# Kernel tuning notes

Hardware: AMD Instinct MI355X
Metric: run time of the kernel (lower is better)

Reference implementation:

```python
import jax, jax.numpy as jnp
import numpy as np
from jax import lax

N = 8388608
HYP2F1_TERMS = 200  # z <= ~0.87 here, 0.87^200 ~ 1e-12 -> fully converged


def hyp2f1(p, q, s, z, n_terms=HYP2F1_TERMS):
    """Gauss 2F1(p, q; s; z) via its power series (|z|<1), fixed-length scan."""
    def step(carry, k):
        term, acc = carry
        term = term * (p + k) * (q + k) / ((s + k) * (k + 1.0)) * z
        return (term, acc + term), None
    ones = jnp.ones_like(z)
    (_, acc), _ = lax.scan(step, (ones, ones),
                           jnp.arange(n_terms, dtype=z.dtype))
    return acc


def setup_inputs() -> dict:
    key = jax.random.key(0)
    k1, k2, k3 = jax.random.split(key, 3)
    x = jax.random.randint(k1, (N,), 0, 20).astype(jnp.int32)
    T = jax.random.uniform(k2, (N,), minval=20.0, maxval=60.0, dtype=jnp.float32)
    u = jax.random.uniform(k3, (N,), dtype=jnp.float32)
    # recency in [0.2*T, 0.9*T] so T - t_x > 0 and z bounded away from 1;
    # t_x = 0 for customers with no repeat transactions (x == 0).
    t_x = jnp.where(x == 0, 0.0, (0.2 + 0.7 * u) * T)
    return {
        "x": x,
        "t_x": t_x,
        "T": T,
        "log_r": jnp.log(jnp.float32(0.9)),
        "log_alpha": jnp.log(jnp.float32(4.0)),
        "log_a": jnp.log(jnp.float32(0.8)),
        "log_b": jnp.log(jnp.float32(2.5)),
    }


def reference(x, t_x, T, log_r, log_alpha, log_a, log_b):
    xf = x.astype(jnp.float32)
    r = jnp.exp(log_r)
    alpha = jnp.exp(log_alpha)
    a = jnp.exp(log_a)
    b = jnp.exp(log_b)

    log_alpha_T = jnp.log(alpha + T)

    # x == 0 branch
    ll0 = r * (jnp.log(alpha) - log_alpha_T) + (jnp.log(b) - jnp.log(a + b))

    # x > 0 branch (safe to evaluate everywhere: T - t_x > 0 for all rows)
    term1 = lax.lgamma(r + xf) - lax.lgamma(r) - lax.lgamma(xf + 1.0)
    term2 = r * (jnp.log(alpha) - log_alpha_T)
    term3 = xf * (jnp.log(T - t_x) - log_alpha_T)
    term4 = (jnp.log(a) + lax.lgamma(a + b) - lax.lgamma(a)
             - lax.lgamma(a + b + xf) + lax.lgamma(a + xf))
    z = (T - t_x) / (alpha + T)
    term5 = jnp.log(hyp2f1(r + xf, a * jnp.ones_like(xf), a + b + xf, z))
    ll1 = term1 + term2 + term3 + term4 + term5

    return jnp.where(x == 0, ll0, ll1)
```

## Files before the change

kernel.cpp:

```cpp
#include <hip/hip_runtime.h>
#include <hip/hip_fp16.h>


#define NX    20
#define MT    64
#define NQ    (MT / 4)
#define ROWH  68
#define BLOB_BYTES (128 + NX * ROWH * 2)

__global__ void bgnbd_setup(const float* __restrict__ plr,
                            const float* __restrict__ pla,
                            const float* __restrict__ plA,
                            const float* __restrict__ plb,
                            float* __restrict__ ws)
{
    const int t = threadIdx.x;
    const float log_r     = plr[0];
    const float log_alpha = pla[0];
    const float log_a     = plA[0];
    const float log_b     = plb[0];
    const float r     = expf(log_r);
    const float a     = expf(log_a);
    const float b     = expf(log_b);
    const float alpha = expf(log_alpha);

    if (t == 0) {
        ws[0] = r;
        ws[1] = log_alpha;
        ws[2] = log_b - logf(a + b);
        ws[3] = alpha;
        ws[4] = 0.f; ws[5] = 0.f; ws[6] = 0.f; ws[7] = 0.f;
        for (int i = 28; i < 32; ++i) ws[i] = 0.f;
    }
    if (t < NX) {
        const float xf = (float)t;
        ws[8 + t] = lgammaf(r + xf) - lgammaf(r) - lgammaf(xf + 1.f)
                  + log_a + lgammaf(a + b) - lgammaf(a)
                  - lgammaf(a + b + xf) + lgammaf(a + xf);
        __half* Dh = reinterpret_cast<__half*>(ws + 32);
        const float p = r + xf;
        const float s = a + b + xf;
        float D = 1.f;
        for (int m = 0; m < MT; ++m) {
            Dh[t * ROWH + m] = __float2half(D);
            const float k = (float)m;
            D = D * (p + k) * (a + k) / ((s + k) * (k + 1.f));
        }
        for (int m = MT; m < ROWH; ++m) Dh[t * ROWH + m] = __float2half(0.f);
    }
}

__global__ __launch_bounds__(256) void bgnbd_main(
    const int*   __restrict__ xp,
    const float* __restrict__ txp,
    const float* __restrict__ Tp,
    const float* __restrict__ ws,
    float*       __restrict__ out,
    int n4)
{
    __shared__ __align__(16) unsigned char blob[BLOB_BYTES];
    const int tid = threadIdx.x;
    {
        const uint4* src = reinterpret_cast<const uint4*>(ws);
        uint4*       dst = reinterpret_cast<uint4*>(blob);
        if (tid < BLOB_BYTES / 16) dst[tid] = src[tid];
    }
    __syncthreads();

    const float*  s_sc = reinterpret_cast<const float*>(blob);
    const float*  s_Cx = s_sc + 8;
    const __half* s_D  = reinterpret_cast<const __half*>(blob + 128);

    const float r         = s_sc[0];
    const float log_alpha = s_sc[1];
    const float ll0c      = s_sc[2];
    const float alpha     = s_sc[3];

    const int gid = blockIdx.x * 256 + tid;
    if (gid >= n4) return;

    const int4   xv  = reinterpret_cast<const int4*>(xp)[gid];
    const float4 txv = reinterpret_cast<const float4*>(txp)[gid];
    const float4 Tv  = reinterpret_cast<const float4*>(Tp)[gid];

    int   xi[4]  = {xv.x, xv.y, xv.z, xv.w};
    float txa[4] = {txv.x, txv.y, txv.z, txv.w};
    float Ta[4]  = {Tv.x, Tv.y, Tv.z, Tv.w};

    float z[4], S[4], lat[4], Tm[4];
    int   xc[4];
    const __half* rowp[4];
    #pragma unroll
    for (int e = 0; e < 4; ++e) {
        const float aT = alpha + Ta[e];
        lat[e] = __logf(aT);
        Tm[e]  = Ta[e] - txa[e];
        z[e]   = __fdividef(Tm[e], aT);
        S[e]   = 0.f;
        int c = xi[e]; c = c < 0 ? 0 : (c > NX - 1 ? NX - 1 : c);
        xc[e]   = c;
        rowp[e] = s_D + c * ROWH;
    }

    #pragma unroll 4
    for (int g = NQ - 1; g >= 0; --g) {
        #pragma unroll
        for (int e = 0; e < 4; ++e) {
            const uint2 q = *reinterpret_cast<const uint2*>(rowp[e] + 4 * g);
            const __half2 h01 = __builtin_bit_cast(__half2, q.x);
            const __half2 h23 = __builtin_bit_cast(__half2, q.y);
            const float2 f01 = __half22float2(h01);
            const float2 f23 = __half22float2(h23);
            S[e] = fmaf(S[e], z[e], f23.y);
            S[e] = fmaf(S[e], z[e], f23.x);
            S[e] = fmaf(S[e], z[e], f01.y);
            S[e] = fmaf(S[e], z[e], f01.x);
        }
    }

    float res[4];
    #pragma unroll
    for (int e = 0; e < 4; ++e) {
        const float base = r * (log_alpha - lat[e]);
        const float xf   = (float)xi[e];
        const float ll1  = s_Cx[xc[e]] + base
                         + xf * (__logf(Tm[e]) - lat[e]) + __logf(S[e]);
        const float ll0  = base + ll0c;
        res[e] = (xi[e] == 0) ? ll0 : ll1;
    }
    reinterpret_cast<float4*>(out)[gid] = make_float4(res[0], res[1], res[2], res[3]);
}

extern "C" void kernel_launch(void* const* d_in, const int* in_sizes, int n_in,
                              void* d_out, int out_size, void* d_ws, size_t ws_size,
                              hipStream_t stream)
{
    const int*   xp  = (const int*)  d_in[0];
    const float* txp = (const float*)d_in[1];
    const float* Tp  = (const float*)d_in[2];
    const float* plr = (const float*)d_in[3];
    const float* pla = (const float*)d_in[4];
    const float* plA = (const float*)d_in[5];
    const float* plb = (const float*)d_in[6];
    float*       out = (float*)d_out;
    float*       ws  = (float*)d_ws;

    const int n  = in_sizes[0];
    const int n4 = n >> 2;
    const int grid = (n4 + 255) / 256;

    bgnbd_setup<<<1, 64, 0, stream>>>(plr, pla, plA, plb, ws);
    bgnbd_main<<<grid, 256, 0, stream>>>(xp, txp, Tp, ws, out, n4);
}
```

Before: 156.9 us.

## Halve hyp2f1 series terms and evaluate pairs with packed fp16 dot2

Cuts the per-element hypergeometric series from 64 to 32 stored coefficients. Evaluates them two at a time with v_dot2 (fdot2) against a packed (1, z) fp16 vector, with a z² Horner step. Folds r*log_alpha into the precomputed constants and moves the final logs to log2 form with a single ln2 rescale. The aim is to remove most of the per-element FMA and convert work in this compute-bound loop. The cost is accuracy: the series is truncated more aggressively, and z is rounded to fp16 inside the dot product.

```diff
diff --git a/kernel.cpp b/kernel.cpp
--- a/kernel.cpp
+++ b/kernel.cpp
@@ -3,10 +3,11 @@
 
 
 #define NX    20
-#define MT    64
-#define NQ    (MT / 4)
-#define ROWH  68
+#define MT    32
+#define ROWH  72
 #define BLOB_BYTES (128 + NX * ROWH * 2)
+
+typedef _Float16 half2_t __attribute__((ext_vector_type(2)));
 
 __global__ void bgnbd_setup(const float* __restrict__ plr,
                             const float* __restrict__ pla,
@@ -26,8 +27,8 @@
 
     if (t == 0) {
         ws[0] = r;
-        ws[1] = log_alpha;
-        ws[2] = log_b - logf(a + b);
+        ws[1] = 0.f;
+        ws[2] = r * log_alpha + log_b - logf(a + b);
         ws[3] = alpha;
         ws[4] = 0.f; ws[5] = 0.f; ws[6] = 0.f; ws[7] = 0.f;
         for (int i = 28; i < 32; ++i) ws[i] = 0.f;
@@ -36,7 +37,8 @@
         const float xf = (float)t;
         ws[8 + t] = lgammaf(r + xf) - lgammaf(r) - lgammaf(xf + 1.f)
                   + log_a + lgammaf(a + b) - lgammaf(a)
-                  - lgammaf(a + b + xf) + lgammaf(a + xf);
+                  - lgammaf(a + b + xf) + lgammaf(a + xf)
+                  + r * log_alpha;
         __half* Dh = reinterpret_cast<__half*>(ws + 32);
         const float p = r + xf;
         const float s = a + b + xf;
@@ -71,10 +73,9 @@
     const float*  s_Cx = s_sc + 8;
     const __half* s_D  = reinterpret_cast<const __half*>(blob + 128);
 
-    const float r         = s_sc[0];
-    const float log_alpha = s_sc[1];
-    const float ll0c      = s_sc[2];
-    const float alpha     = s_sc[3];
+    const float r     = s_sc[0];
+    const float ll0c  = s_sc[2];
+    const float alpha = s_sc[3];
 
     const int gid = blockIdx.x * 256 + tid;
     if (gid >= n4) return;
@@ -87,45 +88,46 @@
     float txa[4] = {txv.x, txv.y, txv.z, txv.w};
     float Ta[4]  = {Tv.x, Tv.y, Tv.z, Tv.w};
 
-    float z[4], S[4], lat[4], Tm[4];
-    int   xc[4];
+    float z[4], w[4], S[4], l2aT[4];
+    half2_t zp[4];
+    int xc[4];
     const __half* rowp[4];
     #pragma unroll
     for (int e = 0; e < 4; ++e) {
         const float aT = alpha + Ta[e];
-        lat[e] = __logf(aT);
-        Tm[e]  = Ta[e] - txa[e];
-        z[e]   = __fdividef(Tm[e], aT);
-        S[e]   = 0.f;
+        l2aT[e] = __log2f(aT);
+        const float Tm = Ta[e] - txa[e];
+        z[e] = __fdividef(Tm, aT);
+        w[e] = z[e] * z[e];
+        const unsigned zh = __half_as_ushort(__float2half(z[e]));
+        zp[e] = __builtin_bit_cast(half2_t, 0x3C00u | (zh << 16));
+        S[e] = 0.f;
         int c = xi[e]; c = c < 0 ? 0 : (c > NX - 1 ? NX - 1 : c);
         xc[e]   = c;
         rowp[e] = s_D + c * ROWH;
     }
 
-    #pragma unroll 4
-    for (int g = NQ - 1; g >= 0; --g) {
+    #pragma unroll
+    for (int j = 3; j >= 0; --j) {
         #pragma unroll
         for (int e = 0; e < 4; ++e) {
-            const uint2 q = *reinterpret_cast<const uint2*>(rowp[e] + 4 * g);
-            const __half2 h01 = __builtin_bit_cast(__half2, q.x);
-            const __half2 h23 = __builtin_bit_cast(__half2, q.y);
-            const float2 f01 = __half22float2(h01);
-            const float2 f23 = __half22float2(h23);
-            S[e] = fmaf(S[e], z[e], f23.y);
-            S[e] = fmaf(S[e], z[e], f23.x);
-            S[e] = fmaf(S[e], z[e], f01.y);
-            S[e] = fmaf(S[e], z[e], f01.x);
+            const uint4 q = *reinterpret_cast<const uint4*>(rowp[e] + 8 * j);
+            S[e] = __builtin_amdgcn_fdot2(__builtin_bit_cast(half2_t, q.w), zp[e], S[e] * w[e], false);
+            S[e] = __builtin_amdgcn_fdot2(__builtin_bit_cast(half2_t, q.z), zp[e], S[e] * w[e], false);
+            S[e] = __builtin_amdgcn_fdot2(__builtin_bit_cast(half2_t, q.y), zp[e], S[e] * w[e], false);
+            S[e] = __builtin_amdgcn_fdot2(__builtin_bit_cast(half2_t, q.x), zp[e], S[e] * w[e], false);
         }
     }
 
+    const float LN2 = 0.69314718055994531f;
     float res[4];
     #pragma unroll
     for (int e = 0; e < 4; ++e) {
-        const float base = r * (log_alpha - lat[e]);
-        const float xf   = (float)xi[e];
-        const float ll1  = s_Cx[xc[e]] + base
-                         + xf * (__logf(Tm[e]) - lat[e]) + __logf(S[e]);
-        const float ll0  = base + ll0c;
+        const float xf  = (float)xi[e];
+        const float b2  = -r * l2aT[e];
+        const float t2  = fmaf(xf, __log2f(z[e]), b2 + __log2f(S[e]));
+        const float ll1 = fmaf(LN2, t2, s_Cx[xc[e]]);
+        const float ll0 = fmaf(LN2, b2, ll0c);
         res[e] = (xi[e] == 0) ? ll0 : ll1;
     }
     reinterpret_cast<float4*>(out)[gid] = make_float4(res[0], res[1], res[2], res[3]);
```

Measured after the change: 144.6 us. 1.09x faster.
